# Kernel tuning notes

Hardware: AMD Instinct MI355X
Metric: run time of the kernel (lower is better)

The kernel has to match this reference:

```python
import jax, jax.numpy as jnp
import numpy as np

D_MODEL = 2048
NUM_HEADS = 16
D_K = D_MODEL // NUM_HEADS


def setup_inputs() -> dict:
    key = jax.random.key(0)
    ks = jax.random.split(key, 9)
    s = 1.0 / np.sqrt(D_MODEL)
    return {
        "x": jax.random.normal(ks[0], (2, 2048, D_MODEL), dtype=jnp.float32),
        "Wq": jax.random.normal(ks[1], (D_MODEL, D_MODEL), dtype=jnp.float32) * s,
        "bq": jax.random.normal(ks[2], (D_MODEL,), dtype=jnp.float32) * 0.01,
        "Wk": jax.random.normal(ks[3], (D_MODEL, D_MODEL), dtype=jnp.float32) * s,
        "bk": jax.random.normal(ks[4], (D_MODEL,), dtype=jnp.float32) * 0.01,
        "Wv": jax.random.normal(ks[5], (D_MODEL, D_MODEL), dtype=jnp.float32) * s,
        "bv": jax.random.normal(ks[6], (D_MODEL,), dtype=jnp.float32) * 0.01,
        "Wo": jax.random.normal(ks[7], (D_MODEL, D_MODEL), dtype=jnp.float32) * s,
        "bo": jax.random.normal(ks[8], (D_MODEL,), dtype=jnp.float32) * 0.01,
    }


def reference(x, Wq, bq, Wk, bk, Wv, bv, Wo, bo):
    B, T, C = x.shape
    H, Dk = NUM_HEADS, D_K
    # projections (torch Linear: y = x @ W^T + b; here weights stored as [in,out])
    q = (x @ Wq + bq).reshape(B, T, H, Dk).transpose(0, 2, 1, 3)  # [B,H,T,Dk]
    k = (x @ Wk + bk).reshape(B, T, H, Dk).transpose(0, 2, 1, 3)
    v = (x @ Wv + bv).reshape(B, T, H, Dk).transpose(0, 2, 1, 3)
    score = jnp.einsum("bhqd,bhkd->bhqk", q, k) / jnp.sqrt(jnp.float32(Dk))
    attn = jax.nn.softmax(score, axis=-1)
    out = jnp.einsum("bhqk,bhkd->bhqd", attn, v)  # [B,H,T,Dk]
    out = out.transpose(0, 2, 1, 3).reshape(B, T, C)
    return out @ Wo + bo
```

## Files before the change

kernel.cpp:

```cpp
#include <hip/hip_runtime.h>
#include <cstdint>

typedef _Float16 f16;
typedef __attribute__((ext_vector_type(4))) _Float16 f16x4;
typedef __attribute__((ext_vector_type(8))) _Float16 f16x8;
typedef __attribute__((ext_vector_type(4))) float f32x4;

#define DM   2048
#define TSEQ 2048
#define NB   2
#define NH   16
#define DKH  128
#define LOG2E 1.44269504088896f

__device__ __forceinline__ void gload_lds16(const void* g, void* l) {
  __builtin_amdgcn_global_load_lds((const __attribute__((address_space(1))) void*)g,
                                   (__attribute__((address_space(3))) void*)l, 16, 0, 0);
}

#define SBAR()  { asm volatile("s_barrier" ::: "memory"); __builtin_amdgcn_sched_barrier(0); }
#define LGKM0() { asm volatile("s_waitcnt lgkmcnt(0)" ::: "memory"); __builtin_amdgcn_sched_barrier(0); }

__global__ __launch_bounds__(256) void cvt_kernel(const float* __restrict__ src,
                                                  f16* __restrict__ dst, int n8) {
  int i = blockIdx.x * 256 + threadIdx.x;
  if (i >= n8) return;
  const float4* s = (const float4*)src + 2 * (size_t)i;
  float4 a = s[0], b = s[1];
  f16x8 o;
  o[0]=(f16)a.x; o[1]=(f16)a.y; o[2]=(f16)a.z; o[3]=(f16)a.w;
  o[4]=(f16)b.x; o[5]=(f16)b.y; o[6]=(f16)b.z; o[7]=(f16)b.w;
  ((f16x8*)dst)[i] = o;
}

__global__ __launch_bounds__(256) void wt_kernel(const float* __restrict__ W0, const float* __restrict__ W1,
                                                 const float* __restrict__ W2, const float* __restrict__ W3,
                                                 f16* __restrict__ Dqkv, f16* __restrict__ Dout) {
  __shared__ f16 S[64 * 80];
  int z = blockIdx.z;
  const float* W = (z == 0) ? W0 : (z == 1) ? W1 : (z == 2) ? W2 : W3;
  f16* D = (z < 3) ? (Dqkv + (size_t)z * DM * DM) : Dout;
  int n0 = blockIdx.x * 64, k0 = blockIdx.y * 64;
  int tid = threadIdx.x;
#pragma unroll
  for (int i = 0; i < 4; i++) {
    int flat = i * 256 + tid;
    int r = flat >> 4, c4 = flat & 15;
    float4 v = *(const float4*)(W + (size_t)(k0 + r) * DM + n0 + c4 * 4);
    S[(c4 * 4 + 0) * 80 + r] = (f16)v.x;
    S[(c4 * 4 + 1) * 80 + r] = (f16)v.y;
    S[(c4 * 4 + 2) * 80 + r] = (f16)v.z;
    S[(c4 * 4 + 3) * 80 + r] = (f16)v.w;
  }
  __syncthreads();
#pragma unroll
  for (int i = 0; i < 2; i++) {
    int flat = i * 256 + tid;
    int nl = flat >> 3, kc = flat & 7;
    f16x8 v = *(const f16x8*)&S[nl * 80 + kc * 8];
    *(f16x8*)(D + (size_t)(n0 + nl) * DM + k0 + kc * 8) = v;
  }
}

template <int MODE>
__global__ __launch_bounds__(512, 2) void gemm_kernel(const f16* __restrict__ A, const f16* __restrict__ Bt,
                                                      const float* __restrict__ b0, const float* __restrict__ b1,
                                                      const float* __restrict__ b2,
                                                      f16* __restrict__ Oh, float* __restrict__ Of) {
  constexpr int BN   = (MODE == 0) ? 192 : 128;
  constexpr int NFR  = BN / 64;
  constexpr int WN   = BN / 4;
  constexpr int NXB  = (MODE == 0) ? 32 : 16;
  constexpr int CPX  = (16 * NXB) / 8;
  __shared__ __align__(16) f16 As[2][256 * 64];
  __shared__ __align__(16) f16 Bs[2][NFR * 64 * 64];
  const int K = DM;
  const int NT = K / 64;
  const int NITER = NT / 2;
  int tid = threadIdx.x, l = tid & 63, w = tid >> 6;
  int lo = l & 15, hi = l >> 4;
  int wm = w >> 2, wn = w & 3;
  int lin = blockIdx.x;
  int swz = (lin & 7) * CPX + (lin >> 3);
  int by = swz & 15, bx = swz >> 4;
  int m0 = by * 256, n0 = bx * BN;

  const f16* Ag = A + (size_t)m0 * K;
  const f16* Bg = Bt + (size_t)n0 * K;

  auto stageAu = [&](int b, int u, int t) {
    int rin = (w << 3) + (l >> 3);
    int csw = (l & 7) ^ (rin & 7);
    gload_lds16(Ag + (size_t)(u * 64 + rin) * K + t * 64 + csw * 8,
                &As[b][u * 4096 + w * 512]);
  };
  auto stageBu = [&](int b, int u, int t) {
    int rin = (w << 3) + (l >> 3);
    int csw = (l & 7) ^ (rin & 7);
    gload_lds16(Bg + (size_t)(u * 64 + rin) * K + t * 64 + csw * 8,
                &Bs[b][u * 4096 + w * 512]);
  };

  f32x4 acc[8][NFR] = {};
  f16x8 bfr[NFR][2];
  f16x8 af[4][2][2];

#define READ_BFRAGS(b)                                                              \
  {                                                                                 \
    _Pragma("unroll")                                                               \
    for (int ni = 0; ni < NFR; ni++) {                                              \
      int row = wn * WN + ni * 16 + lo;                                             \
      bfr[ni][0] = *(const f16x8*)&Bs[b][row * 64 + (((0 + hi) ^ (row & 7)) << 3)]; \
      bfr[ni][1] = *(const f16x8*)&Bs[b][row * 64 + (((4 + hi) ^ (row & 7)) << 3)]; \
    }                                                                               \
  }

#define READ_AFRAGS_ALL(b)                                                          \
  {                                                                                 \
    _Pragma("unroll")                                                               \
    for (int q = 0; q < 4; q++)                                                     \
      _Pragma("unroll")                                                             \
      for (int e = 0; e < 2; e++) {                                                 \
        int row = wm * 128 + (q * 2 + e) * 16 + lo;                                 \
        af[q][e][0] = *(const f16x8*)&As[b][row * 64 + (((0 + hi) ^ (row & 7)) << 3)]; \
        af[q][e][1] = *(const f16x8*)&As[b][row * 64 + (((4 + hi) ^ (row & 7)) << 3)]; \
      }                                                                             \
  }

#define MFMA_Q(q)                                                                   \
    __builtin_amdgcn_s_setprio(1);                                                  \
    _Pragma("unroll")                                                               \
    for (int e = 0; e < 2; e++)                                                     \
      _Pragma("unroll")                                                             \
      for (int ni = 0; ni < NFR; ni++) {                                            \
        acc[(q)*2+e][ni] = __builtin_amdgcn_mfma_f32_16x16x32_f16(af[q][e][0], bfr[ni][0], acc[(q)*2+e][ni], 0, 0, 0); \
        acc[(q)*2+e][ni] = __builtin_amdgcn_mfma_f32_16x16x32_f16(af[q][e][1], bfr[ni][1], acc[(q)*2+e][ni], 0, 0, 0); \
      }                                                                             \
    __builtin_amdgcn_s_setprio(0);

#define VMCNT_UPT()                                                                 \
    if constexpr (MODE == 0) { asm volatile("s_waitcnt vmcnt(7)" ::: "memory"); }   \
    else                     { asm volatile("s_waitcnt vmcnt(6)" ::: "memory"); }   \
    __builtin_amdgcn_sched_barrier(0);

#pragma unroll
  for (int u = 0; u < 4; u++) stageAu(0, u, 0);
#pragma unroll
  for (int u = 0; u < NFR; u++) stageBu(0, u, 0);
#pragma unroll
  for (int u = 0; u < 4; u++) stageAu(1, u, 1);
#pragma unroll
  for (int u = 0; u < NFR; u++) stageBu(1, u, 1);
  VMCNT_UPT();
  SBAR();

#pragma unroll 1
  for (int it = 0; it < NITER; ++it) {
    int t2 = (2 * it + 2 < NT) ? 2 * it + 2 : NT - 1;
    int t3 = (2 * it + 3 < NT) ? 2 * it + 3 : NT - 1;

    {
      READ_BFRAGS(0); READ_AFRAGS_ALL(0);
      MFMA_Q(0);
      SBAR();
    }
    {
      MFMA_Q(1);
      LGKM0();
      SBAR();
    }
    {
#pragma unroll
      for (int u = 0; u < 4; u++) stageAu(0, u, t2);
      MFMA_Q(2);
      SBAR();
    }
    {
#pragma unroll
      for (int u = 0; u < NFR; u++) stageBu(0, u, t2);
      MFMA_Q(3);
      VMCNT_UPT();
      SBAR();
    }

    {
      READ_BFRAGS(1); READ_AFRAGS_ALL(1);
      MFMA_Q(0);
      SBAR();
    }
    {
      MFMA_Q(1);
      LGKM0();
      SBAR();
    }
    {
#pragma unroll
      for (int u = 0; u < 4; u++) stageAu(1, u, t3);
      MFMA_Q(2);
      SBAR();
    }
    {
#pragma unroll
      for (int u = 0; u < NFR; u++) stageBu(1, u, t3);
      MFMA_Q(3);
      VMCNT_UPT();
      SBAR();
    }
  }
  asm volatile("s_waitcnt vmcnt(0)" ::: "memory");

#pragma unroll
  for (int mi = 0; mi < 8; mi++) {
    int gm = m0 + wm * 128 + mi * 16 + (hi << 2);
#pragma unroll
    for (int ni = 0; ni < NFR; ni++) {
      int gn = n0 + wn * WN + ni * 16 + lo;
      if (MODE == 0) {
        int proj = gn >> 11, nn = gn & 2047;
        const float* bp = (proj == 0) ? b0 : (proj == 1) ? b1 : b2;
        float bias = bp[nn];
        int h = nn >> 7, d = nn & 127;
        int b = gm >> 11;
        int t0 = gm & 2047;
        if (proj < 2) {
#pragma unroll
          for (int r = 0; r < 4; r++) {
            Oh[(size_t)proj * ((size_t)NB * NH * TSEQ * DKH) +
               (((size_t)(b * NH + h) * TSEQ + t0 + r) * DKH) + d] = (f16)(acc[mi][ni][r] + bias);
          }
        } else {
          f16x4 pk;
#pragma unroll
          for (int r = 0; r < 4; r++) pk[r] = (f16)(acc[mi][ni][r] + bias);
          *(f16x4*)(Oh + 2ull * ((size_t)NB * NH * TSEQ * DKH) +
                    ((size_t)(b * NH + h) * DKH + d) * TSEQ + t0) = pk;
        }
      } else {
        float bias = b0[gn];
#pragma unroll
        for (int r = 0; r < 4; r++)
          Of[(size_t)(gm + r) * DM + gn] = acc[mi][ni][r] + bias;
      }
    }
  }
#undef READ_BFRAGS
#undef READ_AFRAGS_ALL
#undef MFMA_Q
#undef VMCNT_UPT
}

__global__ __launch_bounds__(256, 2) void attn_kernel(const f16* __restrict__ Qb, const f16* __restrict__ Kb,
                                                      const f16* __restrict__ Vtb, f16* __restrict__ AO) {
  __shared__ f16 Ks[64 * 128];
  __shared__ f16 Vt[128 * 64];
  __shared__ f16 Ps[4][32 * 72];
  int tid = threadIdx.x, l = tid & 63, w = tid >> 6;
  int lo = l & 15, hi = l >> 4;
  int lin = blockIdx.x;
  int xcd = lin & 7, slot = lin >> 3;
  int bh = xcd * 4 + (slot & 3), qt = slot >> 2;
  const float CSC = 0.12753257f;
  const float THR = 62.0f;
  const f16* Qg = Qb + (size_t)bh * TSEQ * DKH;
  const f16* Kg = Kb + (size_t)bh * TSEQ * DKH;
  const f16* Vg = Vtb + (size_t)bh * DKH * TSEQ;

  f16x8 aq[2][4];
#pragma unroll
  for (int hf = 0; hf < 2; hf++) {
    int qrow = qt * 128 + w * 32 + hf * 16 + lo;
#pragma unroll
    for (int c = 0; c < 4; c++)
      aq[hf][c] = *(const f16x8*)(Qg + (size_t)qrow * DKH + c * 32 + (hi << 3));
  }

  f32x4 o[2][8] = {};
  float mrow[2] = {-INFINITY, -INFINITY};
  float lrow[2] = {0.f, 0.f};

  for (int ktile = 0; ktile < TSEQ / 64; ++ktile) {
    __syncthreads();
#pragma unroll
    for (int i = 0; i < 4; i++) {
      int chunk = (w * 4 + i) * 64 + l;
      int rowk = chunk >> 4, c = chunk & 15;
      int csw = c ^ (rowk & 15);
      gload_lds16(Kg + (size_t)(ktile * 64 + rowk) * DKH + csw * 8, &Ks[(w * 4 + i) * 512]);
    }
#pragma unroll
    for (int i = 0; i < 4; i++) {
      int chunk = (w * 4 + i) * 64 + l;
      int d = chunk >> 3, c = chunk & 7;
      int csw = c ^ (d & 7);
      gload_lds16(Vg + (size_t)d * TSEQ + ktile * 64 + csw * 8, &Vt[(w * 4 + i) * 512]);
    }
    __syncthreads();

    f32x4 s[2][4] = {};
    __builtin_amdgcn_s_setprio(1);
#pragma unroll
    for (int ks = 0; ks < 4; ++ks) {
      int ktl = ks * 16 + lo;
#pragma unroll
      for (int c = 0; c < 4; c++) {
        int cc = (c * 4 + hi) ^ lo;
        f16x8 bk = *(const f16x8*)&Ks[ktl * 128 + cc * 8];
        s[0][ks] = __builtin_amdgcn_mfma_f32_16x16x32_f16(bk, aq[0][c], s[0][ks], 0, 0, 0);
        s[1][ks] = __builtin_amdgcn_mfma_f32_16x16x32_f16(bk, aq[1][c], s[1][ks], 0, 0, 0);
      }
    }
    __builtin_amdgcn_s_setprio(0);

#pragma unroll
    for (int hf = 0; hf < 2; hf++) {
      float mk[4];
#pragma unroll
      for (int ks = 0; ks < 4; ks++)
        mk[ks] = fmaxf(fmaxf(s[hf][ks][0], s[hf][ks][1]), fmaxf(s[hf][ks][2], s[hf][ks][3]));
      float mt = fmaxf(fmaxf(mk[0], mk[1]), fmaxf(mk[2], mk[3]));
      mt = fmaxf(mt, __shfl_xor(mt, 16));
      mt = fmaxf(mt, __shfl_xor(mt, 32));

      if (__any(mt > mrow[hf] + THR)) {
        float mn = fmaxf(mrow[hf], mt);
        float al = exp2f((mrow[hf] - mn) * CSC);
        mrow[hf] = mn;
        lrow[hf] *= al;
        float alr[4];
#pragma unroll
        for (int r = 0; r < 4; r++) alr[r] = __shfl(al, (hi << 2) + r);
#pragma unroll
        for (int dsub = 0; dsub < 8; dsub++)
#pragma unroll
          for (int r = 0; r < 4; r++) o[hf][dsub][r] *= alr[r];
      }

      float mCn = -mrow[hf] * CSC;
      float sum = 0.f;
#pragma unroll
      for (int ks = 0; ks < 4; ks++) {
        f16x4 pk;
        float part = 0.f;
#pragma unroll
        for (int r = 0; r < 4; r++) {
          float p = exp2f(__builtin_fmaf(s[hf][ks][r], CSC, mCn));
          pk[r] = (f16)p;
          part += p;
        }
        sum += part;
        *(f16x4*)&Ps[w][(hf * 16 + lo) * 72 + ks * 16 + (hi << 2)] = pk;
      }
      sum += __shfl_xor(sum, 16);
      sum += __shfl_xor(sum, 32);
      lrow[hf] += sum;
    }

    f16x8 pa[2][2];
#pragma unroll
    for (int hf = 0; hf < 2; hf++)
#pragma unroll
      for (int kk = 0; kk < 2; kk++)
        pa[hf][kk] = *(const f16x8*)&Ps[w][(hf * 16 + lo) * 72 + kk * 32 + (hi << 3)];
    __builtin_amdgcn_s_setprio(1);
#pragma unroll
    for (int kk = 0; kk < 2; kk++) {
#pragma unroll
      for (int dsub = 0; dsub < 8; dsub++) {
        int d = dsub * 16 + lo;
        f16x8 vf = *(const f16x8*)&Vt[d * 64 + (((kk * 4 + hi) ^ (d & 7)) << 3)];
        o[0][dsub] = __builtin_amdgcn_mfma_f32_16x16x32_f16(pa[0][kk], vf, o[0][dsub], 0, 0, 0);
        o[1][dsub] = __builtin_amdgcn_mfma_f32_16x16x32_f16(pa[1][kk], vf, o[1][dsub], 0, 0, 0);
      }
    }
    __builtin_amdgcn_s_setprio(0);
  }

  int b = bh >> 4, h = bh & 15;
#pragma unroll
  for (int hf = 0; hf < 2; hf++) {
    float inv = 1.0f / lrow[hf];
    float invr[4];
#pragma unroll
    for (int r = 0; r < 4; r++) invr[r] = __shfl(inv, (hi << 2) + r);
#pragma unroll
    for (int r = 0; r < 4; r++) {
      int t = qt * 128 + w * 32 + hf * 16 + (hi << 2) + r;
      f16* dst = AO + ((size_t)b * TSEQ + t) * DM + h * DKH;
#pragma unroll
      for (int dsub = 0; dsub < 8; dsub++)
        dst[dsub * 16 + lo] = (f16)(o[hf][dsub][r] * invr[r]);
    }
  }
}

extern "C" void kernel_launch(void* const* d_in, const int* in_sizes, int n_in,
                              void* d_out, int out_size, void* d_ws, size_t ws_size,
                              hipStream_t stream) {
  const float* x  = (const float*)d_in[0];
  const float* Wq = (const float*)d_in[1];
  const float* bq = (const float*)d_in[2];
  const float* Wk = (const float*)d_in[3];
  const float* bk = (const float*)d_in[4];
  const float* Wv = (const float*)d_in[5];
  const float* bv = (const float*)d_in[6];
  const float* Wo = (const float*)d_in[7];
  const float* bo = (const float*)d_in[8];

  f16* ws    = (f16*)d_ws;
  f16* xb    = ws;
  f16* WtQKV = ws + 8388608ull;
  f16* WtO   = ws + 20971520ull;
  f16* Q     = ws + 25165824ull;
  f16* Kp    = ws + 33554432ull;
  f16* Vp    = ws + 41943040ull;
  f16* AO    = xb;

  cvt_kernel<<<4096, 256, 0, stream>>>(x, xb, (NB * TSEQ * DM) / 8);
  wt_kernel<<<dim3(32, 32, 4), 256, 0, stream>>>(Wq, Wk, Wv, Wo, WtQKV, WtO);
  gemm_kernel<0><<<512, 512, 0, stream>>>(xb, WtQKV, bq, bk, bv, Q, nullptr);
  attn_kernel<<<512, 256, 0, stream>>>(Q, Kp, Vp, AO);
  gemm_kernel<1><<<256, 512, 0, stream>>>(AO, WtO, bo, nullptr, nullptr, nullptr, (float*)d_out);
}
```

Before: 266.5 us.

## Software-pipeline LDS fragment reads with MFMA and cut barriers in GEMM loop

```diff
diff --git a/kernel.cpp b/kernel.cpp
--- a/kernel.cpp
+++ b/kernel.cpp
@@ -20,6 +20,7 @@
 
 #define SBAR()  { asm volatile("s_barrier" ::: "memory"); __builtin_amdgcn_sched_barrier(0); }
 #define LGKM0() { asm volatile("s_waitcnt lgkmcnt(0)" ::: "memory"); __builtin_amdgcn_sched_barrier(0); }
+#define VMCNT0() { asm volatile("s_waitcnt vmcnt(0)" ::: "memory"); __builtin_amdgcn_sched_barrier(0); }
 
 __global__ __launch_bounds__(256) void cvt_kernel(const float* __restrict__ src,
                                                   f16* __restrict__ dst, int n8) {
@@ -72,6 +73,7 @@
   constexpr int WN   = BN / 4;
   constexpr int NXB  = (MODE == 0) ? 32 : 16;
   constexpr int CPX  = (16 * NXB) / 8;
+  constexpr int UNITS = 4 + NFR;
   __shared__ __align__(16) f16 As[2][256 * 64];
   __shared__ __align__(16) f16 Bs[2][NFR * 64 * 64];
   const int K = DM;
@@ -100,12 +102,18 @@
     gload_lds16(Bg + (size_t)(u * 64 + rin) * K + t * 64 + csw * 8,
                 &Bs[b][u * 4096 + w * 512]);
   };
+  auto stageAll = [&](int b, int t) {
+#pragma unroll
+    for (int u = 0; u < 4; u++) stageAu(b, u, t);
+#pragma unroll
+    for (int u = 0; u < NFR; u++) stageBu(b, u, t);
+  };
 
   f32x4 acc[8][NFR] = {};
   f16x8 bfr[NFR][2];
   f16x8 af[4][2][2];
 
-#define READ_BFRAGS(b)                                                              \
+#define READ_BFR(b)                                                                 \
   {                                                                                 \
     _Pragma("unroll")                                                               \
     for (int ni = 0; ni < NFR; ni++) {                                              \
@@ -115,16 +123,14 @@
     }                                                                               \
   }
 
-#define READ_AFRAGS_ALL(b)                                                          \
+#define READ_AF(b, q)                                                               \
   {                                                                                 \
     _Pragma("unroll")                                                               \
-    for (int q = 0; q < 4; q++)                                                     \
-      _Pragma("unroll")                                                             \
-      for (int e = 0; e < 2; e++) {                                                 \
-        int row = wm * 128 + (q * 2 + e) * 16 + lo;                                 \
-        af[q][e][0] = *(const f16x8*)&As[b][row * 64 + (((0 + hi) ^ (row & 7)) << 3)]; \
-        af[q][e][1] = *(const f16x8*)&As[b][row * 64 + (((4 + hi) ^ (row & 7)) << 3)]; \
-      }                                                                             \
+    for (int e = 0; e < 2; e++) {                                                   \
+      int row = wm * 128 + ((q) * 2 + e) * 16 + lo;                                 \
+      af[q][e][0] = *(const f16x8*)&As[b][row * 64 + (((0 + hi) ^ (row & 7)) << 3)]; \
+      af[q][e][1] = *(const f16x8*)&As[b][row * 64 + (((4 + hi) ^ (row & 7)) << 3)]; \
+    }                                                                               \
   }
 
 #define MFMA_Q(q)                                                                   \
@@ -138,76 +144,45 @@
       }                                                                             \
     __builtin_amdgcn_s_setprio(0);
 
-#define VMCNT_UPT()                                                                 \
+#define VMCNT_P()                                                                   \
     if constexpr (MODE == 0) { asm volatile("s_waitcnt vmcnt(7)" ::: "memory"); }   \
     else                     { asm volatile("s_waitcnt vmcnt(6)" ::: "memory"); }   \
     __builtin_amdgcn_sched_barrier(0);
 
-#pragma unroll
-  for (int u = 0; u < 4; u++) stageAu(0, u, 0);
-#pragma unroll
-  for (int u = 0; u < NFR; u++) stageBu(0, u, 0);
-#pragma unroll
-  for (int u = 0; u < 4; u++) stageAu(1, u, 1);
-#pragma unroll
-  for (int u = 0; u < NFR; u++) stageBu(1, u, 1);
-  VMCNT_UPT();
+  stageAll(0, 0);
+  stageAll(1, 1);
+  VMCNT_P();
   SBAR();
+  READ_BFR(0); READ_AF(0, 0);
 
 #pragma unroll 1
   for (int it = 0; it < NITER; ++it) {
     int t2 = (2 * it + 2 < NT) ? 2 * it + 2 : NT - 1;
     int t3 = (2 * it + 3 < NT) ? 2 * it + 3 : NT - 1;
 
-    {
-      READ_BFRAGS(0); READ_AFRAGS_ALL(0);
-      MFMA_Q(0);
-      SBAR();
-    }
-    {
-      MFMA_Q(1);
-      LGKM0();
-      SBAR();
-    }
-    {
-#pragma unroll
-      for (int u = 0; u < 4; u++) stageAu(0, u, t2);
-      MFMA_Q(2);
-      SBAR();
-    }
-    {
-#pragma unroll
-      for (int u = 0; u < NFR; u++) stageBu(0, u, t2);
-      MFMA_Q(3);
-      VMCNT_UPT();
-      SBAR();
-    }
-
-    {
-      READ_BFRAGS(1); READ_AFRAGS_ALL(1);
-      MFMA_Q(0);
-      SBAR();
-    }
-    {
-      MFMA_Q(1);
-      LGKM0();
-      SBAR();
-    }
-    {
-#pragma unroll
-      for (int u = 0; u < 4; u++) stageAu(1, u, t3);
-      MFMA_Q(2);
-      SBAR();
-    }
-    {
-#pragma unroll
-      for (int u = 0; u < NFR; u++) stageBu(1, u, t3);
-      MFMA_Q(3);
-      VMCNT_UPT();
-      SBAR();
-    }
-  }
-  asm volatile("s_waitcnt vmcnt(0)" ::: "memory");
+    MFMA_Q(0); READ_AF(0, 1);
+    MFMA_Q(1); READ_AF(0, 2);
+    MFMA_Q(2); READ_AF(0, 3);
+    LGKM0();
+    VMCNT0();
+    SBAR();
+    stageAll(0, t2);
+    MFMA_Q(3);
+    __builtin_amdgcn_sched_barrier(0);
+    READ_BFR(1); READ_AF(1, 0);
+
+    MFMA_Q(0); READ_AF(1, 1);
+    MFMA_Q(1); READ_AF(1, 2);
+    MFMA_Q(2); READ_AF(1, 3);
+    LGKM0();
+    VMCNT0();
+    SBAR();
+    stageAll(1, t3);
+    MFMA_Q(3);
+    __builtin_amdgcn_sched_barrier(0);
+    READ_BFR(0); READ_AF(0, 0);
+  }
+  asm volatile("s_waitcnt vmcnt(0) lgkmcnt(0)" ::: "memory");
 
 #pragma unroll
   for (int mi = 0; mi < 8; mi++) {
@@ -243,10 +218,10 @@
       }
     }
   }
-#undef READ_BFRAGS
-#undef READ_AFRAGS_ALL
+#undef READ_BFR
+#undef READ_AF
 #undef MFMA_Q
-#undef VMCNT_UPT
+#undef VMCNT_P
 }
 
 __global__ __launch_bounds__(256, 2) void attn_kernel(const f16* __restrict__ Qb, const f16* __restrict__ Kb,
```

New measurement: 261.9 us. Within noise of the previous version (-1.7%).
